# Kernel tuning notes

Measured on AMD Instinct MI355X. Metric: run time of the kernel, lower is better.

## Reference

```python
import jax, jax.numpy as jnp
import numpy as np

E = 1024
H = 16
HD = E // H  # 64


def setup_inputs() -> dict:
    key = jax.random.key(0)
    ks = jax.random.split(key, 5)
    x = jax.random.normal(ks[0], (2, 2048, E), dtype=jnp.float32)
    s = 1.0 / np.sqrt(E)
    W_qkv = jax.random.uniform(ks[1], (E, 3 * E), jnp.float32, -s, s)
    b_qkv = jax.random.uniform(ks[2], (3 * E,), jnp.float32, -s, s)
    W_out = jax.random.uniform(ks[3], (E, E), jnp.float32, -s, s)
    b_out = jax.random.uniform(ks[4], (E,), jnp.float32, -s, s)
    return {"x": x, "W_qkv": W_qkv, "b_qkv": b_qkv, "W_out": W_out, "b_out": b_out}


def reference(x, W_qkv, b_qkv, W_out, b_out):
    B, N, _ = x.shape
    scale = HD ** (-0.5)
    qkv = x @ W_qkv + b_qkv                         # [B, N, 3E]
    qkv = qkv.reshape(B, N, H, 3 * HD)              # torch layout: per-head 3*hd chunk
    qkv = qkv.transpose(0, 2, 1, 3)                 # [B, H, N, 3*hd]
    q, k, v = jnp.split(qkv, 3, axis=-1)            # each [B, H, N, hd]
    attn = jnp.einsum('bhqd,bhkd->bhqk', q, k) * scale
    attn = jax.nn.softmax(attn, axis=-1)            # dropout is identity in eval
    out = jnp.einsum('bhqk,bhkd->bhqd', attn, v)    # [B, H, N, hd]
    out = out.transpose(0, 2, 1, 3).reshape(B, N, E)
    return out @ W_out + b_out
```

## Files before the change

kernel.cpp:

```cpp
#include <hip/hip_runtime.h>


#define SEQ 2048
#define NH  16

typedef __attribute__((ext_vector_type(8))) short short8;
typedef __attribute__((ext_vector_type(4))) short short4v;
typedef __attribute__((ext_vector_type(4))) float floatx4;
typedef __attribute__((ext_vector_type(4))) _Float16 half4;
typedef __attribute__((ext_vector_type(2))) _Float16 half2v;
typedef __attribute__((ext_vector_type(2))) __fp16 fp16x2;

#define QSCALE 0.1803368801111204f

__device__ __forceinline__ short f2bf(float f) {
    union { float f; unsigned u; } v; v.f = f;
    unsigned r = v.u + 0x7fffu + ((v.u >> 16) & 1u);
    return (short)(r >> 16);
}

__device__ __forceinline__ float fast_exp2(float x) {
#if __has_builtin(__builtin_amdgcn_exp2f)
    return __builtin_amdgcn_exp2f(x);
#else
    return exp2f(x);
#endif
}

__device__ __forceinline__ half2v cvt_pk(float a, float b) {
#if __has_builtin(__builtin_amdgcn_cvt_pkrtz)
    union { fp16x2 i; half2v o; } u;
    u.i = __builtin_amdgcn_cvt_pkrtz(a, b);
    return u.o;
#else
    half2v r; r.x = (_Float16)a; r.y = (_Float16)b; return r;
#endif
}

#define GLDS16(gp, lp)                                                          \
    __builtin_amdgcn_global_load_lds(                                           \
        (const __attribute__((address_space(1))) unsigned int*)(gp),            \
        (__attribute__((address_space(3))) unsigned int*)(lp), 16, 0, 0)

__global__ __launch_bounds__(256) void cast_f32_bf16_kernel(
    const float* __restrict__ in, short* __restrict__ out)
{
    int i = blockIdx.x * 256 + threadIdx.x;
    const float4* in4 = (const float4*)in + (size_t)i * 2;
    float4 a = in4[0], b = in4[1];
    short8 o = { f2bf(a.x), f2bf(a.y), f2bf(a.z), f2bf(a.w),
                 f2bf(b.x), f2bf(b.y), f2bf(b.z), f2bf(b.w) };
    *((short8*)out + i) = o;
}

__global__ __launch_bounds__(256) void transpose_cast_kernel(
    const float* __restrict__ in, short* __restrict__ out, int R, int C)
{
    __shared__ float T[64][65];
    const int tid = threadIdx.x;
    const int c0 = blockIdx.x * 64, r0 = blockIdx.y * 64;
#pragma unroll
    for (int it = 0; it < 4; ++it) {
        int r = it * 16 + (tid >> 4), c = (tid & 15) * 4;
        float4 v = *(const float4*)(in + (size_t)(r0 + r) * C + c0 + c);
        T[c+0][r] = v.x; T[c+1][r] = v.y; T[c+2][r] = v.z; T[c+3][r] = v.w;
    }
    __syncthreads();
#pragma unroll
    for (int it = 0; it < 4; ++it) {
        int oc = it * 16 + (tid >> 4), k = (tid & 15) * 4;
        short4v o = { f2bf(T[oc][k]), f2bf(T[oc][k+1]), f2bf(T[oc][k+2]), f2bf(T[oc][k+3]) };
        *(short4v*)(out + (size_t)(c0 + oc) * R + r0 + k) = o;
    }
}

__global__ __launch_bounds__(256) void vtrans_kernel(
    const _Float16* __restrict__ vn, _Float16* __restrict__ vt)
{
    __shared__ _Float16 T[64][72];
    const int tid = threadIdx.x;
    const int bh = blockIdx.y, n0 = blockIdx.x * 64;
#pragma unroll
    for (int it = 0; it < 2; ++it) {
        int n = it * 32 + (tid >> 3), c = (tid & 7) * 8;
        const _Float16* p = vn + ((size_t)bh * SEQ + n0 + n) * 64 + c;
        half4 a = *(const half4*)(p);
        half4 b = *(const half4*)(p + 4);
        T[c+0][n] = a.x; T[c+1][n] = a.y; T[c+2][n] = a.z; T[c+3][n] = a.w;
        T[c+4][n] = b.x; T[c+5][n] = b.y; T[c+6][n] = b.z; T[c+7][n] = b.w;
    }
    __syncthreads();
#pragma unroll
    for (int it = 0; it < 2; ++it) {
        int idx = it * 256 + tid;
        int quad = idx & 3, d = (idx >> 2) & 63, u = idx >> 8;
        const _Float16* row = &T[d][u * 32 + quad * 4];
        half4 lo = *(const half4*)(row);
        half4 hi = *(const half4*)(row + 16);
        _Float16* q = vt + ((size_t)bh * 64 + d) * SEQ + n0 + u * 32 + quad * 8;
        *(half4*)(q)     = lo;
        *(half4*)(q + 4) = hi;
    }
}

#define GEMM_CORE(A_PTR, B_PTR, LDA, LDB)                                        \
    __shared__ short As[128 * 32];                                               \
    __shared__ short Bs[128 * 32];                                               \
    const int tid  = threadIdx.x;                                                \
    const int lane = tid & 63, w = tid >> 6;                                     \
    const int quad = lane >> 4, l16 = lane & 15;                                 \
    const int wm = w >> 1, wn = w & 1;                                           \
    const int c0 = blockIdx.x * 128, r0 = blockIdx.y * 128;                      \
    floatx4 acc[4][4];                                                           \
    _Pragma("unroll")                                                            \
    for (int i = 0; i < 4; ++i)                                                  \
        _Pragma("unroll")                                                        \
        for (int j = 0; j < 4; ++j) acc[i][j] = (floatx4){0.f, 0.f, 0.f, 0.f};   \
    const int srow = tid >> 2;                                                   \
    const int sgx  = ((tid & 3) ^ ((srow >> 1) & 3)) * 8;                        \
    const short* Ag = (A_PTR) + (size_t)(r0 + srow) * (LDA) + sgx;               \
    const short* Bg = (B_PTR) + (size_t)(c0 + srow) * (LDB) + sgx;               \
    const int fsw = (l16 >> 1) & 3;                                              \
    for (int kk = 0; kk < 1024; kk += 32) {                                      \
        __syncthreads();                                                         \
        GLDS16(Ag + kk,                      As + tid * 8);                      \
        GLDS16(Ag + (size_t)64 * (LDA) + kk, As + 2048 + tid * 8);               \
        GLDS16(Bg + kk,                      Bs + tid * 8);                      \
        GLDS16(Bg + (size_t)64 * (LDB) + kk, Bs + 2048 + tid * 8);               \
        __syncthreads();                                                         \
        short8 af[4], bf[4];                                                     \
        _Pragma("unroll")                                                        \
        for (int mt = 0; mt < 4; ++mt)                                           \
            af[mt] = *(const short8*)&As[(wm * 64 + mt * 16 + l16) * 32 + (quad ^ fsw) * 8]; \
        _Pragma("unroll")                                                        \
        for (int nt = 0; nt < 4; ++nt)                                           \
            bf[nt] = *(const short8*)&Bs[(wn * 64 + nt * 16 + l16) * 32 + (quad ^ fsw) * 8]; \
        _Pragma("unroll")                                                        \
        for (int mt = 0; mt < 4; ++mt)                                           \
            _Pragma("unroll")                                                    \
            for (int nt = 0; nt < 4; ++nt)                                       \
                acc[mt][nt] = __builtin_amdgcn_mfma_f32_16x16x32_bf16(           \
                    af[mt], bf[nt], acc[mt][nt], 0, 0, 0);                       \
    }

__global__ __launch_bounds__(256) void qkv_gemm_kernel(
    const short* __restrict__ wt, const short* __restrict__ xb,
    const float* __restrict__ bias,
    short* __restrict__ qb, short* __restrict__ kb, _Float16* __restrict__ vnb)
{
    GEMM_CORE(wt, xb, 1024, 1024)
#pragma unroll
    for (int mt = 0; mt < 4; ++mt) {
        int oc0 = r0 + wm * 64 + mt * 16 + quad * 4;
        int head = oc0 / 192;
        int t = (oc0 - head * 192) >> 6;
        int d0 = oc0 & 63;
        float4 bv = *(const float4*)(bias + oc0);
#pragma unroll
        for (int nt = 0; nt < 4; ++nt) {
            int tok = c0 + wn * 64 + nt * 16 + l16;
            int bh = (tok >> 11) * NH + head;
            size_t base = ((size_t)bh * SEQ + (tok & (SEQ - 1))) * 64 + d0;
            float v0 = acc[mt][nt][0] + bv.x, v1 = acc[mt][nt][1] + bv.y;
            float v2 = acc[mt][nt][2] + bv.z, v3 = acc[mt][nt][3] + bv.w;
            if (t == 0) {
                short4v o = { f2bf(v0 * QSCALE), f2bf(v1 * QSCALE),
                              f2bf(v2 * QSCALE), f2bf(v3 * QSCALE) };
                *(short4v*)(qb + base) = o;
            } else if (t == 1) {
                short4v o = { f2bf(v0), f2bf(v1), f2bf(v2), f2bf(v3) };
                *(short4v*)(kb + base) = o;
            } else {
                half4 o = { (_Float16)v0, (_Float16)v1, (_Float16)v2, (_Float16)v3 };
                *(half4*)(vnb + base) = o;
            }
        }
    }
}

__global__ __launch_bounds__(512) void out_gemm_kernel(
    const short* __restrict__ wt, const short* __restrict__ ab,
    const float* __restrict__ bias, float* __restrict__ out)
{
    __shared__ short As[128 * 32];
    __shared__ short Bs[128 * 32];
    const int tid  = threadIdx.x;
    const int lane = tid & 63, w = tid >> 6;
    const int quad = lane >> 4, l16 = lane & 15;
    const int wm = w >> 2, wn = w & 3;
    const int c0 = blockIdx.x * 128, r0 = blockIdx.y * 128;
    floatx4 acc[4][2];
#pragma unroll
    for (int i = 0; i < 4; ++i)
#pragma unroll
        for (int j = 0; j < 2; ++j) acc[i][j] = (floatx4){0.f, 0.f, 0.f, 0.f};
    const int srow = tid >> 2;
    const int sgx  = ((tid & 3) ^ ((srow >> 1) & 3)) * 8;
    const short* Ag = wt + (size_t)(r0 + srow) * 1024 + sgx;
    const short* Bg = ab + (size_t)(c0 + srow) * 1024 + sgx;
    const int fsw = (l16 >> 1) & 3;
    for (int kk = 0; kk < 1024; kk += 32) {
        __syncthreads();
        GLDS16(Ag + kk, As + tid * 8);
        GLDS16(Bg + kk, Bs + tid * 8);
        __syncthreads();
        short8 af[4], bf[2];
#pragma unroll
        for (int mt = 0; mt < 4; ++mt)
            af[mt] = *(const short8*)&As[(wm * 64 + mt * 16 + l16) * 32 + (quad ^ fsw) * 8];
#pragma unroll
        for (int nt = 0; nt < 2; ++nt)
            bf[nt] = *(const short8*)&Bs[(wn * 32 + nt * 16 + l16) * 32 + (quad ^ fsw) * 8];
#pragma unroll
        for (int mt = 0; mt < 4; ++mt)
#pragma unroll
            for (int nt = 0; nt < 2; ++nt)
                acc[mt][nt] = __builtin_amdgcn_mfma_f32_16x16x32_bf16(
                    af[mt], bf[nt], acc[mt][nt], 0, 0, 0);
    }
#pragma unroll
    for (int mt = 0; mt < 4; ++mt) {
        int oc0 = r0 + wm * 64 + mt * 16 + quad * 4;
        float4 bv = *(const float4*)(bias + oc0);
#pragma unroll
        for (int nt = 0; nt < 2; ++nt) {
            int tok = c0 + wn * 32 + nt * 16 + l16;
            float4 o = { acc[mt][nt][0] + bv.x, acc[mt][nt][1] + bv.y,
                         acc[mt][nt][2] + bv.z, acc[mt][nt][3] + bv.w };
            *(float4*)(out + (size_t)tok * 1024 + oc0) = o;
        }
    }
}

__global__ __launch_bounds__(256) void attn_kernel(
    const short* __restrict__ qb, const short* __restrict__ kb,
    const _Float16* __restrict__ vtb, short* __restrict__ ob)
{
    __shared__ short    Ks[128 * 64];
    __shared__ _Float16 Vts[64 * 128];
    __shared__ float    Ls[4][64];
    const int tid  = threadIdx.x;
    const int lane = tid & 63, w = tid >> 6;
    const int quad = lane >> 4, l16 = lane & 15;
    const int bh = blockIdx.x;
    const int q0 = blockIdx.y * 64;

    short8 aq[4][2];
#pragma unroll
    for (int qf = 0; qf < 4; ++qf) {
        const short* qp = qb + ((size_t)bh * SEQ + q0 + qf * 16 + l16) * 64 + quad * 8;
        aq[qf][0] = *(const short8*)(qp);
        aq[qf][1] = *(const short8*)(qp + 32);
    }

    const int krow = tid >> 3, kg = tid & 7;
    const short* kgp = kb + ((size_t)bh * SEQ + krow) * 64 + (kg ^ (krow & 7)) * 8;
    const _Float16* vgp = vtb + ((size_t)bh * 64 + (tid >> 2)) * SEQ + (tid & 3) * 8;

    floatx4 o_acc[4][4];
#pragma unroll
    for (int dt = 0; dt < 4; ++dt)
#pragma unroll
        for (int qf = 0; qf < 4; ++qf) o_acc[dt][qf] = (floatx4){0.f, 0.f, 0.f, 0.f};
    float lw[4] = {0.f, 0.f, 0.f, 0.f};

    for (int k0 = 0; k0 < SEQ; k0 += 128) {
        __syncthreads();
        const short* kc_p = kgp + (size_t)k0 * 64;
        GLDS16(kc_p,        Ks + tid * 8);
        GLDS16(kc_p + 2048, Ks + 2048 + tid * 8);
        GLDS16(kc_p + 4096, Ks + 4096 + tid * 8);
        GLDS16(kc_p + 6144, Ks + 6144 + tid * 8);
        const _Float16* vc_p = vgp + k0;
        GLDS16((const short*)(vc_p),      (short*)Vts + tid * 8);
        GLDS16((const short*)(vc_p + 32), (short*)Vts + 2048 + tid * 8);
        GLDS16((const short*)(vc_p + 64), (short*)Vts + 4096 + tid * 8);
        GLDS16((const short*)(vc_p + 96), (short*)Vts + 6144 + tid * 8);
        __syncthreads();

        half4 avlo[4], avhi[4];
#pragma unroll
        for (int dt = 0; dt < 4; ++dt) {
            union { short8 s; struct { half4 lo; half4 hi; } h; } u;
            u.s = *(const short8*)((const short*)Vts + w * 2048 + (dt * 16 + l16) * 32 + quad * 8);
            avlo[dt] = u.h.lo; avhi[dt] = u.h.hi;
        }

#pragma unroll
        for (int kt = 0; kt < 2; ++kt) {
            const short* krp = &Ks[(w * 32 + kt * 16 + l16) * 64];
            short8 ak0 = *(const short8*)(krp + ((0 + quad) ^ (l16 & 7)) * 8);
            short8 ak1 = *(const short8*)(krp + ((4 + quad) ^ (l16 & 7)) * 8);
            floatx4 sacc[4];
#pragma unroll
            for (int qf = 0; qf < 4; ++qf) {
                floatx4 z = (floatx4){0.f, 0.f, 0.f, 0.f};
                z = __builtin_amdgcn_mfma_f32_16x16x32_bf16(ak0, aq[qf][0], z, 0, 0, 0);
                sacc[qf] = __builtin_amdgcn_mfma_f32_16x16x32_bf16(ak1, aq[qf][1], z, 0, 0, 0);
            }
            half4 pf[4];
#pragma unroll
            for (int qf = 0; qf < 4; ++qf) {
                float p0 = fast_exp2(sacc[qf][0]);
                float p1 = fast_exp2(sacc[qf][1]);
                float p2 = fast_exp2(sacc[qf][2]);
                float p3 = fast_exp2(sacc[qf][3]);
                lw[qf] += (p0 + p1) + (p2 + p3);
                half2v lo = cvt_pk(p0, p1), hi = cvt_pk(p2, p3);
                pf[qf] = (half4){lo.x, lo.y, hi.x, hi.y};
            }
#pragma unroll
            for (int dt = 0; dt < 4; ++dt)
#pragma unroll
                for (int qf = 0; qf < 4; ++qf)
                    o_acc[dt][qf] = __builtin_amdgcn_mfma_f32_16x16x16f16(
                        kt ? avhi[dt] : avlo[dt], pf[qf], o_acc[dt][qf], 0, 0, 0);
        }
    }

#pragma unroll
    for (int qf = 0; qf < 4; ++qf) {
        lw[qf] += __shfl_xor(lw[qf], 16);
        lw[qf] += __shfl_xor(lw[qf], 32);
        if (quad == 0) Ls[w][qf * 16 + l16] = lw[qf];
    }

    float* RedA = (float*)Ks;
    float* RedB = (float*)Vts;
    __syncthreads();
#pragma unroll
    for (int dt = 0; dt < 4; ++dt)
#pragma unroll
        for (int qf = 0; qf < 4; ++qf) {
            int fi = (((dt * 4 + qf) * 4 + quad) * 16 + l16) * 4;
            if (w == 1) *(floatx4*)&RedA[fi] = o_acc[dt][qf];
            if (w == 3) *(floatx4*)&RedB[fi] = o_acc[dt][qf];
        }
    __syncthreads();
    if (w == 0 || w == 2) {
#pragma unroll
        for (int dt = 0; dt < 4; ++dt)
#pragma unroll
            for (int qf = 0; qf < 4; ++qf) {
                int fi = (((dt * 4 + qf) * 4 + quad) * 16 + l16) * 4;
                o_acc[dt][qf] += *(const floatx4*)((w == 0) ? &RedA[fi] : &RedB[fi]);
                if (w == 2) *(floatx4*)&RedB[fi] = o_acc[dt][qf];
            }
    }
    __syncthreads();
    if (w == 0) {
        float inv[4];
#pragma unroll
        for (int qf = 0; qf < 4; ++qf) {
            int qi = qf * 16 + l16;
            inv[qf] = 1.0f / (Ls[0][qi] + Ls[1][qi] + Ls[2][qi] + Ls[3][qi]);
        }
        const int b = bh >> 4, h = bh & 15;
#pragma unroll
        for (int dt = 0; dt < 4; ++dt)
#pragma unroll
            for (int qf = 0; qf < 4; ++qf) {
                int fi = (((dt * 4 + qf) * 4 + quad) * 16 + l16) * 4;
                floatx4 o = o_acc[dt][qf] + *(const floatx4*)&RedB[fi];
                int tok = b * SEQ + q0 + qf * 16 + l16;
                short4v o4 = { f2bf(o[0] * inv[qf]), f2bf(o[1] * inv[qf]),
                               f2bf(o[2] * inv[qf]), f2bf(o[3] * inv[qf]) };
                *(short4v*)(ob + (size_t)tok * 1024 + h * 64 + dt * 16 + quad * 4) = o4;
            }
    }
}

extern "C" void kernel_launch(void* const* d_in, const int* in_sizes, int n_in,
                              void* d_out, int out_size, void* d_ws, size_t ws_size,
                              hipStream_t stream) {
    const float* x     = (const float*)d_in[0];
    const float* W_qkv = (const float*)d_in[1];
    const float* b_qkv = (const float*)d_in[2];
    const float* W_out = (const float*)d_in[3];
    const float* b_out = (const float*)d_in[4];
    float* out = (float*)d_out;

    short* xb      = (short*)d_ws;
    short* wqkvt   = xb    + (size_t)4096 * 1024;
    short* woutt   = wqkvt + (size_t)3072 * 1024;
    short* qb      = woutt + (size_t)1024 * 1024;
    short* kb      = qb    + (size_t)32 * SEQ * 64;
    _Float16* vnb  = (_Float16*)(kb + (size_t)32 * SEQ * 64);
    _Float16* vtb  = vnb + (size_t)32 * SEQ * 64;
    short* ob      = (short*)(vtb + (size_t)32 * 64 * SEQ);

    cast_f32_bf16_kernel<<<2048, 256, 0, stream>>>(x, xb);
    transpose_cast_kernel<<<dim3(48, 16), 256, 0, stream>>>(W_qkv, wqkvt, 1024, 3072);
    transpose_cast_kernel<<<dim3(16, 16), 256, 0, stream>>>(W_out, woutt, 1024, 1024);
    qkv_gemm_kernel<<<dim3(32, 24), 256, 0, stream>>>(wqkvt, xb, b_qkv, qb, kb, vnb);
    vtrans_kernel<<<dim3(32, 32), 256, 0, stream>>>(vnb, vtb);
    attn_kernel<<<dim3(32, 32), 256, 0, stream>>>(qb, kb, vtb, ob);
    out_gemm_kernel<<<dim3(32, 8), 512, 0, stream>>>(woutt, ob, b_out, out);
}
```

Baseline: 207.0 us.

## Split attention block into 8 waves over query halves with swizzled V tile

The attention kernel moves from 4 to 8 waves per block. Each group of four waves handles 32 of the 64 queries, and within a group the waves split the 128-key chunk. Cooperative K/V loads now take two loads per thread instead of four, and the V^T shared-memory tile gets an XOR swizzle to cut bank conflicts on reads. This halves accumulator registers per wave to raise parallelism and latency hiding. In exchange, the same K/V tile is read by twice as many waves and the block is larger.

```diff
diff --git a/kernel.cpp b/kernel.cpp
--- a/kernel.cpp
+++ b/kernel.cpp
@@ -232,75 +232,75 @@
     }
 }
 
-__global__ __launch_bounds__(256) void attn_kernel(
+__global__ __launch_bounds__(512) void attn_kernel(
     const short* __restrict__ qb, const short* __restrict__ kb,
     const _Float16* __restrict__ vtb, short* __restrict__ ob)
 {
     __shared__ short    Ks[128 * 64];
     __shared__ _Float16 Vts[64 * 128];
-    __shared__ float    Ls[4][64];
+    __shared__ float    Ls[8][32];
     const int tid  = threadIdx.x;
     const int lane = tid & 63, w = tid >> 6;
     const int quad = lane >> 4, l16 = lane & 15;
+    const int qh = w >> 2, kq = w & 3;
     const int bh = blockIdx.x;
     const int q0 = blockIdx.y * 64;
 
-    short8 aq[4][2];
-#pragma unroll
-    for (int qf = 0; qf < 4; ++qf) {
-        const short* qp = qb + ((size_t)bh * SEQ + q0 + qf * 16 + l16) * 64 + quad * 8;
+    short8 aq[2][2];
+#pragma unroll
+    for (int qf = 0; qf < 2; ++qf) {
+        const short* qp = qb + ((size_t)bh * SEQ + q0 + qh * 32 + qf * 16 + l16) * 64 + quad * 8;
         aq[qf][0] = *(const short8*)(qp);
         aq[qf][1] = *(const short8*)(qp + 32);
     }
 
     const int krow = tid >> 3, kg = tid & 7;
     const short* kgp = kb + ((size_t)bh * SEQ + krow) * 64 + (kg ^ (krow & 7)) * 8;
-    const _Float16* vgp = vtb + ((size_t)bh * 64 + (tid >> 2)) * SEQ + (tid & 3) * 8;
-
-    floatx4 o_acc[4][4];
+    const int vd = (tid >> 2) & 63, vgg = tid & 3, vu = tid >> 8;
+    const _Float16* vgp = vtb + ((size_t)bh * 64 + vd) * SEQ + vu * 32
+                        + (vgg ^ ((vd >> 1) & 3)) * 8;
+
+    floatx4 o_acc[4][2];
 #pragma unroll
     for (int dt = 0; dt < 4; ++dt)
 #pragma unroll
-        for (int qf = 0; qf < 4; ++qf) o_acc[dt][qf] = (floatx4){0.f, 0.f, 0.f, 0.f};
-    float lw[4] = {0.f, 0.f, 0.f, 0.f};
+        for (int qf = 0; qf < 2; ++qf) o_acc[dt][qf] = (floatx4){0.f, 0.f, 0.f, 0.f};
+    float lw[2] = {0.f, 0.f};
 
     for (int k0 = 0; k0 < SEQ; k0 += 128) {
         __syncthreads();
         const short* kc_p = kgp + (size_t)k0 * 64;
         GLDS16(kc_p,        Ks + tid * 8);
-        GLDS16(kc_p + 2048, Ks + 2048 + tid * 8);
         GLDS16(kc_p + 4096, Ks + 4096 + tid * 8);
-        GLDS16(kc_p + 6144, Ks + 6144 + tid * 8);
         const _Float16* vc_p = vgp + k0;
         GLDS16((const short*)(vc_p),      (short*)Vts + tid * 8);
-        GLDS16((const short*)(vc_p + 32), (short*)Vts + 2048 + tid * 8);
         GLDS16((const short*)(vc_p + 64), (short*)Vts + 4096 + tid * 8);
-        GLDS16((const short*)(vc_p + 96), (short*)Vts + 6144 + tid * 8);
         __syncthreads();
 
         half4 avlo[4], avhi[4];
 #pragma unroll
         for (int dt = 0; dt < 4; ++dt) {
             union { short8 s; struct { half4 lo; half4 hi; } h; } u;
-            u.s = *(const short8*)((const short*)Vts + w * 2048 + (dt * 16 + l16) * 32 + quad * 8);
+            u.s = *(const short8*)((const short*)Vts + kq * 2048
+                    + (dt * 16 + l16) * 32 + (quad ^ ((l16 >> 1) & 3)) * 8);
             avlo[dt] = u.h.lo; avhi[dt] = u.h.hi;
         }
 
 #pragma unroll
         for (int kt = 0; kt < 2; ++kt) {
-            const short* krp = &Ks[(w * 32 + kt * 16 + l16) * 64];
+            const short* krp = &Ks[(kq * 32 + kt * 16 + l16) * 64];
             short8 ak0 = *(const short8*)(krp + ((0 + quad) ^ (l16 & 7)) * 8);
             short8 ak1 = *(const short8*)(krp + ((4 + quad) ^ (l16 & 7)) * 8);
-            floatx4 sacc[4];
-#pragma unroll
-            for (int qf = 0; qf < 4; ++qf) {
+            floatx4 sacc[2];
+#pragma unroll
+            for (int qf = 0; qf < 2; ++qf) {
                 floatx4 z = (floatx4){0.f, 0.f, 0.f, 0.f};
                 z = __builtin_amdgcn_mfma_f32_16x16x32_bf16(ak0, aq[qf][0], z, 0, 0, 0);
                 sacc[qf] = __builtin_amdgcn_mfma_f32_16x16x32_bf16(ak1, aq[qf][1], z, 0, 0, 0);
             }
-            half4 pf[4];
-#pragma unroll
-            for (int qf = 0; qf < 4; ++qf) {
+            half4 pf[2];
+#pragma unroll
+            for (int qf = 0; qf < 2; ++qf) {
                 float p0 = fast_exp2(sacc[qf][0]);
                 float p1 = fast_exp2(sacc[qf][1]);
                 float p2 = fast_exp2(sacc[qf][2]);
@@ -312,14 +312,14 @@
 #pragma unroll
             for (int dt = 0; dt < 4; ++dt)
 #pragma unroll
-                for (int qf = 0; qf < 4; ++qf)
+                for (int qf = 0; qf < 2; ++qf)
                     o_acc[dt][qf] = __builtin_amdgcn_mfma_f32_16x16x16f16(
                         kt ? avhi[dt] : avlo[dt], pf[qf], o_acc[dt][qf], 0, 0, 0);
         }
     }
 
 #pragma unroll
-    for (int qf = 0; qf < 4; ++qf) {
+    for (int qf = 0; qf < 2; ++qf) {
         lw[qf] += __shfl_xor(lw[qf], 16);
         lw[qf] += __shfl_xor(lw[qf], 32);
         if (quad == 0) Ls[w][qf * 16 + l16] = lw[qf];
@@ -331,38 +331,39 @@
 #pragma unroll
     for (int dt = 0; dt < 4; ++dt)
 #pragma unroll
-        for (int qf = 0; qf < 4; ++qf) {
-            int fi = (((dt * 4 + qf) * 4 + quad) * 16 + l16) * 4;
-            if (w == 1) *(floatx4*)&RedA[fi] = o_acc[dt][qf];
-            if (w == 3) *(floatx4*)&RedB[fi] = o_acc[dt][qf];
+        for (int qf = 0; qf < 2; ++qf) {
+            int fi = (((qh * 2 + qf) * 4 + dt) * 64 + lane) * 4;
+            if (kq == 2) *(floatx4*)&RedA[fi] = o_acc[dt][qf];
+            if (kq == 3) *(floatx4*)&RedB[fi] = o_acc[dt][qf];
         }
     __syncthreads();
-    if (w == 0 || w == 2) {
+    if (kq == 0 || kq == 1) {
 #pragma unroll
         for (int dt = 0; dt < 4; ++dt)
 #pragma unroll
-            for (int qf = 0; qf < 4; ++qf) {
-                int fi = (((dt * 4 + qf) * 4 + quad) * 16 + l16) * 4;
-                o_acc[dt][qf] += *(const floatx4*)((w == 0) ? &RedA[fi] : &RedB[fi]);
-                if (w == 2) *(floatx4*)&RedB[fi] = o_acc[dt][qf];
+            for (int qf = 0; qf < 2; ++qf) {
+                int fi = (((qh * 2 + qf) * 4 + dt) * 64 + lane) * 4;
+                o_acc[dt][qf] += *(const floatx4*)((kq == 0) ? &RedA[fi] : &RedB[fi]);
+                if (kq == 1) *(floatx4*)&RedB[fi] = o_acc[dt][qf];
             }
     }
     __syncthreads();
-    if (w == 0) {
-        float inv[4];
-#pragma unroll
-        for (int qf = 0; qf < 4; ++qf) {
+    if (kq == 0) {
+        float inv[2];
+#pragma unroll
+        for (int qf = 0; qf < 2; ++qf) {
             int qi = qf * 16 + l16;
-            inv[qf] = 1.0f / (Ls[0][qi] + Ls[1][qi] + Ls[2][qi] + Ls[3][qi]);
+            inv[qf] = 1.0f / (Ls[qh * 4 + 0][qi] + Ls[qh * 4 + 1][qi]
+                            + Ls[qh * 4 + 2][qi] + Ls[qh * 4 + 3][qi]);
         }
         const int b = bh >> 4, h = bh & 15;
 #pragma unroll
         for (int dt = 0; dt < 4; ++dt)
 #pragma unroll
-            for (int qf = 0; qf < 4; ++qf) {
-                int fi = (((dt * 4 + qf) * 4 + quad) * 16 + l16) * 4;
+            for (int qf = 0; qf < 2; ++qf) {
+                int fi = (((qh * 2 + qf) * 4 + dt) * 64 + lane) * 4;
                 floatx4 o = o_acc[dt][qf] + *(const floatx4*)&RedB[fi];
-                int tok = b * SEQ + q0 + qf * 16 + l16;
+                int tok = b * SEQ + q0 + qh * 32 + qf * 16 + l16;
                 short4v o4 = { f2bf(o[0] * inv[qf]), f2bf(o[1] * inv[qf]),
                                f2bf(o[2] * inv[qf]), f2bf(o[3] * inv[qf]) };
                 *(short4v*)(ob + (size_t)tok * 1024 + h * 64 + dt * 16 + quad * 4) = o4;
@@ -394,6 +395,6 @@
     transpose_cast_kernel<<<dim3(16, 16), 256, 0, stream>>>(W_out, woutt, 1024, 1024);
     qkv_gemm_kernel<<<dim3(32, 24), 256, 0, stream>>>(wqkvt, xb, b_qkv, qb, kb, vnb);
     vtrans_kernel<<<dim3(32, 32), 256, 0, stream>>>(vnb, vtb);
-    attn_kernel<<<dim3(32, 32), 256, 0, stream>>>(qb, kb, vtb, ob);
+    attn_kernel<<<dim3(32, 32), 512, 0, stream>>>(qb, kb, vtb, ob);
     out_gemm_kernel<<<dim3(32, 8), 512, 0, stream>>>(woutt, ob, b_out, out);
 }
```

Result: no change. 207.0 us (+0.0%).
